# Kernel optimization log

Measured on AMD Instinct MI355X. Metric: run time of the kernel, lower is better.

The kernel has to match this reference:

```python
import jax, jax.numpy as jnp
import numpy as np

B, T, I, H = 64, 512, 512, 512

def setup_inputs() -> dict:
    key = jax.random.key(0)
    ks = jax.random.split(key, 13)
    s = 0.02
    return {
        'inputs': jax.random.normal(ks[0], (B, T, I), dtype=jnp.float32),
        'W_i': jax.random.normal(ks[1], (I, H), dtype=jnp.float32) * s,
        'W_f': jax.random.normal(ks[2], (I, H), dtype=jnp.float32) * s,
        'W_o': jax.random.normal(ks[3], (I, H), dtype=jnp.float32) * s,
        'W_c': jax.random.normal(ks[4], (I, H), dtype=jnp.float32) * s,
        'U_i': jax.random.normal(ks[5], (H, H), dtype=jnp.float32) * s,
        'U_f': jax.random.normal(ks[6], (H, H), dtype=jnp.float32) * s,
        'U_o': jax.random.normal(ks[7], (H, H), dtype=jnp.float32) * s,
        'U_c': jax.random.normal(ks[8], (H, H), dtype=jnp.float32) * s,
        'b_i': jax.random.normal(ks[9], (1, H), dtype=jnp.float32) * s,
        'b_f': jax.random.normal(ks[10], (1, H), dtype=jnp.float32) * s,
        'b_o': jax.random.normal(ks[11], (1, H), dtype=jnp.float32) * s,
        'b_c': jax.random.normal(ks[12], (1, H), dtype=jnp.float32) * s,
    }

def reference(inputs, W_i, W_f, W_o, W_c, U_i, U_f, U_o, U_c, b_i, b_f, b_o, b_c):
    batch = inputs.shape[0]
    hidden = U_i.shape[0]
    # Precompute input projections for all 4 gates in one fused GEMM: [T, B, 4H]
    W = jnp.concatenate([W_i, W_f, W_o, W_c], axis=1)          # [I, 4H]
    b = jnp.concatenate([b_i, b_f, b_o, b_c], axis=1)          # [1, 4H]
    U = jnp.concatenate([U_i, U_f, U_o, U_c], axis=1)          # [H, 4H]
    x_proj = jnp.einsum('bti,ig->tbg', inputs, W) + b          # [T, B, 4H]

    def step(carry, xg):
        h, c = carry
        g = xg + h @ U                                          # [B, 4H]
        i_g = jax.nn.sigmoid(g[:, 0*hidden:1*hidden])
        f_g = jax.nn.sigmoid(g[:, 1*hidden:2*hidden])
        o_g = jax.nn.sigmoid(g[:, 2*hidden:3*hidden])
        c_t = jnp.tanh(g[:, 3*hidden:4*hidden])
        c = f_g * c + i_g * c_t
        h = o_g * jnp.tanh(c)
        return (h, c), None

    h0 = jnp.zeros((batch, hidden), dtype=inputs.dtype)
    c0 = jnp.zeros((batch, hidden), dtype=inputs.dtype)
    (h, c), _ = jax.lax.scan(step, (h0, c0), x_proj)
    return h
```

## Files before the change

### kernel.cpp

```cpp
#include <hip/hip_runtime.h>
#include <hip/hip_bf16.h>
#include <cstdint>


typedef __bf16 bf16;
typedef __bf16 bf16x8 __attribute__((ext_vector_type(8)));
typedef float floatx4 __attribute__((ext_vector_type(4)));
typedef uint64_t u64;
typedef uint32_t u32;

#define T_STEPS 512

#define XP_OFF     0ull
#define XBF_OFF    134217728ull
#define WCT_OFF    167772160ull
#define USW_OFF    169869312ull
#define BCAT_OFF   171966464ull
#define HBUF_OFF   171974656ull

__device__ inline u32 pack_bf16x2(float a, float b) {
    union { __bf16 h[2]; u32 u; } cv;
    cv.h[0] = (__bf16)a; cv.h[1] = (__bf16)b;
    return cv.u;
}
__device__ inline float bf_lo(u32 w) { return __builtin_bit_cast(float, w << 16); }
__device__ inline float bf_hi(u32 w) { return __builtin_bit_cast(float, w & 0xffff0000u); }

__device__ inline void lgkm_barrier() {
    __atomic_signal_fence(__ATOMIC_SEQ_CST);
    __builtin_amdgcn_s_waitcnt(0xc07f);
    __builtin_amdgcn_s_barrier();
    __atomic_signal_fence(__ATOMIC_SEQ_CST);
}

__global__ void k0a_convert(const float* __restrict__ in, bf16* __restrict__ xbf) {
    int o = blockIdx.x * 256 + threadIdx.x;
    int k = o & 511;
    int r = o >> 9;
    int t = r >> 6, b = r & 63;
    xbf[o] = (bf16)in[(b * 512 + t) * 512 + k];
}

__global__ void k0b_wcat(const float* __restrict__ Wi, const float* __restrict__ Wf,
                         const float* __restrict__ Wo, const float* __restrict__ Wc,
                         const float* __restrict__ bi, const float* __restrict__ bfv,
                         const float* __restrict__ bo, const float* __restrict__ bc,
                         bf16* __restrict__ wct, float* __restrict__ bcat) {
    int o = blockIdx.x * 256 + threadIdx.x;
    int k = o & 511;
    int c = o >> 9;
    int h = c >> 2, g = c & 3;
    const float* W = (g == 0) ? Wi : (g == 1) ? Wf : (g == 2) ? Wo : Wc;
    wct[o] = (bf16)W[k * 512 + h];
    if (o < 2048) {
        int hh = o >> 2, gg = o & 3;
        const float* bv = (gg == 0) ? bi : (gg == 1) ? bfv : (gg == 2) ? bo : bc;
        bcat[o] = bv[hh];
    }
}

__global__ void k0c_uswz(const float* __restrict__ Ui, const float* __restrict__ Uf,
                         const float* __restrict__ Uo, const float* __restrict__ Uc,
                         bf16* __restrict__ usw) {
    int o = blockIdx.x * 256 + threadIdx.x;
    int e  = o & 7;
    int l  = (o >> 3) & 63;
    int ks = (o >> 9) & 15;
    int nt = (o >> 13) & 1;
    int w  = (o >> 14) & 3;
    int s  = o >> 16;
    int k = ks * 32 + (l >> 4) * 8 + e;
    int col_local = (2 * w + nt) * 16 + (l & 15);
    int h = s * 32 + (col_local >> 2);
    int g = col_local & 3;
    const float* U = (g == 0) ? Ui : (g == 1) ? Uf : (g == 2) ? Uo : Uc;
    usw[o] = (bf16)U[k * 512 + h];
}

__launch_bounds__(256, 2)
__global__ void k1_gemm(const bf16* __restrict__ xbf, const bf16* __restrict__ wct,
                        const float* __restrict__ bcat, bf16* __restrict__ xp) {
    __shared__ bf16 As[128 * 40];
    __shared__ bf16 Bs[128 * 40];
    int tid = threadIdx.x;
    int wid = tid >> 6, lane = tid & 63;
    int q = lane >> 4, m = lane & 15;
    int wr = wid >> 1, wc = wid & 1;
    int br = blockIdx.x & 255, bc = blockIdx.x >> 8;

    floatx4 acc[4][4] = {};

    for (int kk = 0; kk < 16; ++kk) {
        #pragma unroll
        for (int cc = 0; cc < 2; ++cc) {
            int ch = tid + cc * 256;
            int row = ch >> 2, part = ch & 3;
            bf16x8 va = *(const bf16x8*)&xbf[(br * 128 + row) * 512 + kk * 32 + part * 8];
            bf16x8 vb = *(const bf16x8*)&wct[(bc * 128 + row) * 512 + kk * 32 + part * 8];
            *(bf16x8*)&As[row * 40 + part * 8] = va;
            *(bf16x8*)&Bs[row * 40 + part * 8] = vb;
        }
        __syncthreads();
        bf16x8 af[4], bfr[4];
        #pragma unroll
        for (int i = 0; i < 4; ++i) {
            af[i]  = *(const bf16x8*)&As[(wr * 64 + i * 16 + m) * 40 + q * 8];
            bfr[i] = *(const bf16x8*)&Bs[(wc * 64 + i * 16 + m) * 40 + q * 8];
        }
        #pragma unroll
        for (int mt = 0; mt < 4; ++mt)
            #pragma unroll
            for (int nt = 0; nt < 4; ++nt)
                acc[mt][nt] = __builtin_amdgcn_mfma_f32_16x16x32_bf16(
                    af[mt], bfr[nt], acc[mt][nt], 0, 0, 0);
        __syncthreads();
    }
    float bias[4];
    #pragma unroll
    for (int nt = 0; nt < 4; ++nt) bias[nt] = bcat[bc * 128 + wc * 64 + nt * 16 + m];
    #pragma unroll
    for (int mt = 0; mt < 4; ++mt) {
        #pragma unroll
        for (int nt = 0; nt < 4; ++nt) {
            u32 p0 = pack_bf16x2(acc[mt][nt][0] + bias[nt], acc[mt][nt][1] + bias[nt]);
            u32 p1 = pack_bf16x2(acc[mt][nt][2] + bias[nt], acc[mt][nt][3] + bias[nt]);
            size_t idx = (((((size_t)(br * 2 + wr) * 4 + mt) * 16 + bc) * 8
                           + wc * 4 + nt) * 64 + lane) * 4;
            uint2 v; v.x = p0; v.y = p1;
            *(uint2*)&xp[idx] = v;
        }
    }
}

__launch_bounds__(256, 1)
__global__ void k2_rec(const bf16* __restrict__ xp, const bf16* __restrict__ usw,
                       u64* __restrict__ hbuf, float* __restrict__ out) {
    __shared__ bf16 h_lds[16 * 520];
    __shared__ float g_lds[16 * 136];
    u32* h32 = (u32*)h_lds;

    int tid = threadIdx.x;
    int wid = tid >> 6, lane = tid & 63;
    int q = lane >> 4, m = lane & 15;
    int bg = blockIdx.x & 3, s = blockIdx.x >> 2;

    bf16x8 bfr[2][16];
    {
        const bf16x8* base = (const bf16x8*)usw;
        #pragma unroll
        for (int nt = 0; nt < 2; ++nt)
            #pragma unroll
            for (int ks = 0; ks < 16; ++ks)
                bfr[nt][ks] = base[(((s * 4 + wid) * 2 + nt) * 16 + ks) * 64 + lane];
    }

    int r = tid >> 4;
    int jc = (tid & 15) * 2;
    float cs0 = 0.f, cs1 = 0.f;

    uint2 vx0, vx1;
    {
        size_t b0 = ((((size_t)bg * 16 + s) * 8 + wid * 2) * 64 + lane) * 4;
        vx0 = *(const uint2*)&xp[b0];
        vx1 = *(const uint2*)&xp[b0 + 256];
    }

    for (int t = 0; t < T_STEPS; ++t) {
        floatx4 acc[2];

        acc[0][0] = bf_lo(vx0.x); acc[0][1] = bf_hi(vx0.x);
        acc[0][2] = bf_lo(vx0.y); acc[0][3] = bf_hi(vx0.y);
        acc[1][0] = bf_lo(vx1.x); acc[1][1] = bf_hi(vx1.x);
        acc[1][2] = bf_lo(vx1.y); acc[1][3] = bf_hi(vx1.y);

        if (t > 0) {
            __atomic_signal_fence(__ATOMIC_SEQ_CST);
            __builtin_amdgcn_s_sleep(8);
            __atomic_signal_fence(__ATOMIC_SEQ_CST);

            const u64* rb = hbuf + ((size_t)((t - 1) & 1) * 4 + bg) * 4096;
            u32 tg = (u32)t;
            u64 w[16];
            #pragma unroll
            for (int i = 0; i < 16; ++i)
                w[i] = __hip_atomic_load(rb + tid + 256 * i, __ATOMIC_RELAXED,
                                         __HIP_MEMORY_SCOPE_AGENT);
            for (;;) {
                bool ok = true;
                #pragma unroll
                for (int i = 0; i < 16; ++i) ok &= ((u32)(w[i] >> 32) == tg);
                if (ok) break;
                #pragma unroll
                for (int i = 0; i < 16; ++i)
                    w[i] = __hip_atomic_load(rb + tid + 256 * i, __ATOMIC_RELAXED,
                                             __HIP_MEMORY_SCOPE_AGENT);
            }
            #pragma unroll
            for (int i = 0; i < 16; ++i)
                h32[i * 260 + tid] = (u32)w[i];
            lgkm_barrier();
            #pragma unroll
            for (int ks = 0; ks < 16; ++ks) {
                bf16x8 af = *(const bf16x8*)&h_lds[m * 520 + ks * 32 + q * 8];
                acc[0] = __builtin_amdgcn_mfma_f32_16x16x32_bf16(af, bfr[0][ks], acc[0], 0, 0, 0);
                acc[1] = __builtin_amdgcn_mfma_f32_16x16x32_bf16(af, bfr[1][ks], acc[1], 0, 0, 0);
            }
        }

        if (t + 1 < T_STEPS) {
            size_t b0 = (((((size_t)(t + 1) * 4 + bg) * 16 + s) * 8 + wid * 2) * 64 + lane) * 4;
            vx0 = *(const uint2*)&xp[b0];
            vx1 = *(const uint2*)&xp[b0 + 256];
        }

        #pragma unroll
        for (int nt = 0; nt < 2; ++nt) {
            int col = (2 * wid + nt) * 16 + m;
            #pragma unroll
            for (int rr = 0; rr < 4; ++rr)
                g_lds[(q * 4 + rr) * 136 + col] = acc[nt][rr];
        }
        lgkm_barrier();

        floatx4 ga = *(const floatx4*)&g_lds[r * 136 + jc * 4];
        floatx4 gb = *(const floatx4*)&g_lds[r * 136 + jc * 4 + 4];
        float h0, h1;
        {
            float ig = 1.f / (1.f + __expf(-ga[0]));
            float fg = 1.f / (1.f + __expf(-ga[1]));
            float og = 1.f / (1.f + __expf(-ga[2]));
            float th = 1.f - 2.f / (__expf(2.f * ga[3]) + 1.f);
            cs0 = fg * cs0 + ig * th;
            h0 = og * (1.f - 2.f / (__expf(2.f * cs0) + 1.f));
        }
        {
            float ig = 1.f / (1.f + __expf(-gb[0]));
            float fg = 1.f / (1.f + __expf(-gb[1]));
            float og = 1.f / (1.f + __expf(-gb[2]));
            float th = 1.f - 2.f / (__expf(2.f * gb[3]) + 1.f);
            cs1 = fg * cs1 + ig * th;
            h1 = og * (1.f - 2.f / (__expf(2.f * cs1) + 1.f));
        }
        u64 word = ((u64)(u32)(t + 1) << 32) | (u64)pack_bf16x2(h0, h1);
        __hip_atomic_store(hbuf + (((size_t)(t & 1) * 4 + bg) * 16 + r) * 256
                                + s * 16 + (tid & 15),
                           word, __ATOMIC_RELAXED, __HIP_MEMORY_SCOPE_AGENT);
        if (t == T_STEPS - 1) {
            out[(bg * 16 + r) * 512 + s * 32 + jc]     = h0;
            out[(bg * 16 + r) * 512 + s * 32 + jc + 1] = h1;
        }
    }
}

extern "C" void kernel_launch(void* const* d_in, const int* in_sizes, int n_in,
                              void* d_out, int out_size, void* d_ws, size_t ws_size,
                              hipStream_t stream) {
    const float* inp = (const float*)d_in[0];
    const float* Wi  = (const float*)d_in[1];
    const float* Wf  = (const float*)d_in[2];
    const float* Wo  = (const float*)d_in[3];
    const float* Wc  = (const float*)d_in[4];
    const float* Ui  = (const float*)d_in[5];
    const float* Uf  = (const float*)d_in[6];
    const float* Uo  = (const float*)d_in[7];
    const float* Uc  = (const float*)d_in[8];
    const float* bi  = (const float*)d_in[9];
    const float* bfv = (const float*)d_in[10];
    const float* bo  = (const float*)d_in[11];
    const float* bc  = (const float*)d_in[12];

    char* ws = (char*)d_ws;
    bf16*  xp    = (bf16*)(ws + XP_OFF);
    bf16*  xbf   = (bf16*)(ws + XBF_OFF);
    bf16*  wct   = (bf16*)(ws + WCT_OFF);
    bf16*  usw   = (bf16*)(ws + USW_OFF);
    float* bcat  = (float*)(ws + BCAT_OFF);
    u64*   hbuf  = (u64*)(ws + HBUF_OFF);

    k0a_convert<<<65536, 256, 0, stream>>>(inp, xbf);
    k0b_wcat<<<4096, 256, 0, stream>>>(Wi, Wf, Wo, Wc, bi, bfv, bo, bc, wct, bcat);
    k0c_uswz<<<4096, 256, 0, stream>>>(Ui, Uf, Uo, Uc, usw);
    k1_gemm<<<4096, 256, 0, stream>>>(xbf, wct, bcat, xp);
    k2_rec<<<64, 256, 0, stream>>>(xp, usw, hbuf, (float*)d_out);
}
```

Measured before the change: 1.426 ms.

## Poll hidden state with sc0 inline-asm loads and fall back to an agent-scope mirror buffer

The recurrent kernel now waits for other blocks' hidden state with a tight polling loop. The loop uses inline-asm global loads carrying the sc0 cache bit and a very short sleep. If the data does not arrive within a bounded number of tries, the block permanently switches to the old sleep-and-atomic-load path on a second mirrored buffer. Each step now stores h twice (a plain store plus an atomic store to the mirror). The grid is doubled so that, with half the blocks exiting at once, the remaining 64 blocks are likely spread across different XCDs or CUs. This adds store traffic and depends on cache-coherence behaviour of sc0 loads across XCDs, which may be fragile.

```diff
diff --git a/kernel.cpp b/kernel.cpp
--- a/kernel.cpp
+++ b/kernel.cpp
@@ -10,6 +10,7 @@
 typedef uint32_t u32;
 
 #define T_STEPS 512
+#define FAST_TRIES 512
 
 #define XP_OFF     0ull
 #define XBF_OFF    134217728ull
@@ -17,6 +18,7 @@
 #define USW_OFF    169869312ull
 #define BCAT_OFF   171966464ull
 #define HBUF_OFF   171974656ull
+#define HBUF2_OFF  172236800ull
 
 __device__ inline u32 pack_bf16x2(float a, float b) {
     union { __bf16 h[2]; u32 u; } cv;
@@ -132,9 +134,45 @@
     }
 }
 
+#define POLL_ISSUE(base_)                                                         \
+    asm volatile(                                                                 \
+        "global_load_dwordx2 %[w0],  %[o0], %[sb] sc0\n\t"                        \
+        "global_load_dwordx2 %[w1],  %[o0], %[sb] offset:2048 sc0\n\t"            \
+        "global_load_dwordx2 %[w2],  %[o1], %[sb] sc0\n\t"                        \
+        "global_load_dwordx2 %[w3],  %[o1], %[sb] offset:2048 sc0\n\t"            \
+        "global_load_dwordx2 %[w4],  %[o2], %[sb] sc0\n\t"                        \
+        "global_load_dwordx2 %[w5],  %[o2], %[sb] offset:2048 sc0\n\t"            \
+        "global_load_dwordx2 %[w6],  %[o3], %[sb] sc0\n\t"                        \
+        "global_load_dwordx2 %[w7],  %[o3], %[sb] offset:2048 sc0\n\t"            \
+        "global_load_dwordx2 %[w8],  %[o4], %[sb] sc0\n\t"                        \
+        "global_load_dwordx2 %[w9],  %[o4], %[sb] offset:2048 sc0\n\t"            \
+        "global_load_dwordx2 %[w10], %[o5], %[sb] sc0\n\t"                        \
+        "global_load_dwordx2 %[w11], %[o5], %[sb] offset:2048 sc0\n\t"            \
+        "global_load_dwordx2 %[w12], %[o6], %[sb] sc0\n\t"                        \
+        "global_load_dwordx2 %[w13], %[o6], %[sb] offset:2048 sc0\n\t"            \
+        "global_load_dwordx2 %[w14], %[o7], %[sb] sc0\n\t"                        \
+        "global_load_dwordx2 %[w15], %[o7], %[sb] offset:2048 sc0\n\t"            \
+        "s_waitcnt vmcnt(0)"                                                      \
+        : [w0] "=&v"(w[0]),  [w1] "=&v"(w[1]),  [w2] "=&v"(w[2]),                 \
+          [w3] "=&v"(w[3]),  [w4] "=&v"(w[4]),  [w5] "=&v"(w[5]),                 \
+          [w6] "=&v"(w[6]),  [w7] "=&v"(w[7]),  [w8] "=&v"(w[8]),                 \
+          [w9] "=&v"(w[9]),  [w10] "=&v"(w[10]), [w11] "=&v"(w[11]),              \
+          [w12] "=&v"(w[12]), [w13] "=&v"(w[13]), [w14] "=&v"(w[14]),             \
+          [w15] "=&v"(w[15])                                                      \
+        : [o0] "v"(voff[0]), [o1] "v"(voff[1]), [o2] "v"(voff[2]),                \
+          [o3] "v"(voff[3]), [o4] "v"(voff[4]), [o5] "v"(voff[5]),                \
+          [o6] "v"(voff[6]), [o7] "v"(voff[7]), [sb] "s"(base_)                   \
+        : "memory")
+
 __launch_bounds__(256, 1)
 __global__ void k2_rec(const bf16* __restrict__ xp, const bf16* __restrict__ usw,
-                       u64* __restrict__ hbuf, float* __restrict__ out) {
+                       u64* __restrict__ hbuf, u64* __restrict__ hbuf2,
+                       float* __restrict__ out) {
+    int bid = blockIdx.x;
+    if ((bid & 7) >= 4) return;
+    int bg = bid & 7;
+    int s  = bid >> 3;
+
     __shared__ bf16 h_lds[16 * 520];
     __shared__ float g_lds[16 * 136];
     u32* h32 = (u32*)h_lds;
@@ -142,7 +180,6 @@
     int tid = threadIdx.x;
     int wid = tid >> 6, lane = tid & 63;
     int q = lane >> 4, m = lane & 15;
-    int bg = blockIdx.x & 3, s = blockIdx.x >> 2;
 
     bf16x8 bfr[2][16];
     {
@@ -157,6 +194,12 @@
     int r = tid >> 4;
     int jc = (tid & 15) * 2;
     float cs0 = 0.f, cs1 = 0.f;
+
+    u32 voff[8];
+    #pragma unroll
+    for (int j = 0; j < 8; ++j) voff[j] = (u32)(tid * 8 + j * 4096);
+
+    bool fast_mode = true;
 
     uint2 vx0, vx1;
     {
@@ -174,26 +217,45 @@
         acc[1][2] = bf_lo(vx1.y); acc[1][3] = bf_hi(vx1.y);
 
         if (t > 0) {
-            __atomic_signal_fence(__ATOMIC_SEQ_CST);
-            __builtin_amdgcn_s_sleep(8);
-            __atomic_signal_fence(__ATOMIC_SEQ_CST);
-
-            const u64* rb = hbuf + ((size_t)((t - 1) & 1) * 4 + bg) * 4096;
+            u64 w[16];
             u32 tg = (u32)t;
-            u64 w[16];
-            #pragma unroll
-            for (int i = 0; i < 16; ++i)
-                w[i] = __hip_atomic_load(rb + tid + 256 * i, __ATOMIC_RELAXED,
-                                         __HIP_MEMORY_SCOPE_AGENT);
-            for (;;) {
-                bool ok = true;
-                #pragma unroll
-                for (int i = 0; i < 16; ++i) ok &= ((u32)(w[i] >> 32) == tg);
-                if (ok) break;
+            bool have = false;
+            size_t roff = ((size_t)((t - 1) & 1) * 4 + bg) * 4096;
+
+            if (fast_mode) {
+                u64 rbase = (u64)(uintptr_t)(hbuf + roff);
+                int tries = FAST_TRIES;
+                POLL_ISSUE(rbase);
+                for (;;) {
+                    bool ok = true;
+                    #pragma unroll
+                    for (int i = 0; i < 16; ++i) ok &= ((u32)(w[i] >> 32) == tg);
+                    if (ok) { have = true; break; }
+                    if (--tries == 0) break;
+                    __builtin_amdgcn_s_sleep(1);
+                    POLL_ISSUE(rbase);
+                }
+                if (!have) fast_mode = false;
+            }
+            if (!have) {
+                __atomic_signal_fence(__ATOMIC_SEQ_CST);
+                __builtin_amdgcn_s_sleep(8);
+                __atomic_signal_fence(__ATOMIC_SEQ_CST);
+                const u64* rb = hbuf2 + roff;
                 #pragma unroll
                 for (int i = 0; i < 16; ++i)
                     w[i] = __hip_atomic_load(rb + tid + 256 * i, __ATOMIC_RELAXED,
                                              __HIP_MEMORY_SCOPE_AGENT);
+                for (;;) {
+                    bool ok = true;
+                    #pragma unroll
+                    for (int i = 0; i < 16; ++i) ok &= ((u32)(w[i] >> 32) == tg);
+                    if (ok) break;
+                    #pragma unroll
+                    for (int i = 0; i < 16; ++i)
+                        w[i] = __hip_atomic_load(rb + tid + 256 * i, __ATOMIC_RELAXED,
+                                                 __HIP_MEMORY_SCOPE_AGENT);
+                }
             }
             #pragma unroll
             for (int i = 0; i < 16; ++i)
@@ -242,9 +304,11 @@
             h1 = og * (1.f - 2.f / (__expf(2.f * cs1) + 1.f));
         }
         u64 word = ((u64)(u32)(t + 1) << 32) | (u64)pack_bf16x2(h0, h1);
-        __hip_atomic_store(hbuf + (((size_t)(t & 1) * 4 + bg) * 16 + r) * 256
-                                + s * 16 + (tid & 15),
-                           word, __ATOMIC_RELAXED, __HIP_MEMORY_SCOPE_AGENT);
+        size_t widx = (((size_t)(t & 1) * 4 + bg) * 16 + r) * 256
+                      + s * 16 + (tid & 15);
+        hbuf[widx] = word;
+        __hip_atomic_store(hbuf2 + widx, word, __ATOMIC_RELAXED,
+                           __HIP_MEMORY_SCOPE_AGENT);
         if (t == T_STEPS - 1) {
             out[(bg * 16 + r) * 512 + s * 32 + jc]     = h0;
             out[(bg * 16 + r) * 512 + s * 32 + jc + 1] = h1;
@@ -276,10 +340,11 @@
     bf16*  usw   = (bf16*)(ws + USW_OFF);
     float* bcat  = (float*)(ws + BCAT_OFF);
     u64*   hbuf  = (u64*)(ws + HBUF_OFF);
+    u64*   hbuf2 = (u64*)(ws + HBUF2_OFF);
 
     k0a_convert<<<65536, 256, 0, stream>>>(inp, xbf);
     k0b_wcat<<<4096, 256, 0, stream>>>(Wi, Wf, Wo, Wc, bi, bfv, bo, bc, wct, bcat);
     k0c_uswz<<<4096, 256, 0, stream>>>(Ui, Uf, Uo, Uc, usw);
     k1_gemm<<<4096, 256, 0, stream>>>(xbf, wct, bcat, xp);
-    k2_rec<<<64, 256, 0, stream>>>(xp, usw, hbuf, (float*)d_out);
-}
+    k2_rec<<<128, 256, 0, stream>>>(xp, usw, hbuf, hbuf2, (float*)d_out);
+}
```

Result: slower. 4.114 ms (+188.4%).

## Use per-wave gate slabs, double-buffered swizzled h LDS, drop a block barrier

Applied to the files above, without the earlier changes.

Each wave now writes its own gate outputs into a private LDS slab and computes its own cell updates, so the second block-wide barrier per timestep becomes a wave-local LDS fence. The h buffer in LDS is double-buffered by timestep parity, which makes it safe to drop that barrier, and it uses an XOR swizzle instead of padding to avoid bank conflicts. Work per thread is remapped to match, and the hbuf store and output indices change accordingly. The aim is to shorten the serial per-step critical path of the recurrence, at the risk of getting the new index mapping wrong.

```diff
diff --git a/kernel.cpp b/kernel.cpp
--- a/kernel.cpp
+++ b/kernel.cpp
@@ -30,6 +30,13 @@
     __atomic_signal_fence(__ATOMIC_SEQ_CST);
     __builtin_amdgcn_s_waitcnt(0xc07f);
     __builtin_amdgcn_s_barrier();
+    __atomic_signal_fence(__ATOMIC_SEQ_CST);
+}
+
+__device__ inline void wave_lds_fence() {
+    __atomic_signal_fence(__ATOMIC_SEQ_CST);
+    __builtin_amdgcn_s_waitcnt(0xc07f);
+    __builtin_amdgcn_sched_barrier(0);
     __atomic_signal_fence(__ATOMIC_SEQ_CST);
 }
 
@@ -135,9 +142,8 @@
 __launch_bounds__(256, 1)
 __global__ void k2_rec(const bf16* __restrict__ xp, const bf16* __restrict__ usw,
                        u64* __restrict__ hbuf, float* __restrict__ out) {
-    __shared__ bf16 h_lds[16 * 520];
-    __shared__ float g_lds[16 * 136];
-    u32* h32 = (u32*)h_lds;
+    __shared__ u32 h_sh[2][16 * 256];
+    __shared__ float g_slab[4][16 * 36];
 
     int tid = threadIdx.x;
     int wid = tid >> 6, lane = tid & 63;
@@ -154,9 +160,13 @@
                 bfr[nt][ks] = base[(((s * 4 + wid) * 2 + nt) * 16 + ks) * 64 + lane];
     }
 
-    int r = tid >> 4;
-    int jc = (tid & 15) * 2;
+    int r2 = lane >> 2;
+    int kk2 = lane & 3;
     float cs0 = 0.f, cs1 = 0.f;
+
+    int wc = tid >> 2, wk = tid & 3;
+
+    float* gs = &g_slab[wid][0];
 
     uint2 vx0, vx1;
     {
@@ -195,13 +205,15 @@
                     w[i] = __hip_atomic_load(rb + tid + 256 * i, __ATOMIC_RELAXED,
                                              __HIP_MEMORY_SCOPE_AGENT);
             }
+            u32* hp = &h_sh[(t & 1) ^ 1][0];
             #pragma unroll
             for (int i = 0; i < 16; ++i)
-                h32[i * 260 + tid] = (u32)w[i];
+                hp[i * 256 + ((wc ^ (i & 7)) << 2) + wk] = (u32)w[i];
             lgkm_barrier();
+            const bf16* hbs = (const bf16*)hp;
             #pragma unroll
             for (int ks = 0; ks < 16; ++ks) {
-                bf16x8 af = *(const bf16x8*)&h_lds[m * 520 + ks * 32 + q * 8];
+                bf16x8 af = *(const bf16x8*)&hbs[m * 512 + (((4 * ks + q) ^ (m & 7)) << 3)];
                 acc[0] = __builtin_amdgcn_mfma_f32_16x16x32_bf16(af, bfr[0][ks], acc[0], 0, 0, 0);
                 acc[1] = __builtin_amdgcn_mfma_f32_16x16x32_bf16(af, bfr[1][ks], acc[1], 0, 0, 0);
             }
@@ -214,16 +226,14 @@
         }
 
         #pragma unroll
-        for (int nt = 0; nt < 2; ++nt) {
-            int col = (2 * wid + nt) * 16 + m;
+        for (int nt = 0; nt < 2; ++nt)
             #pragma unroll
             for (int rr = 0; rr < 4; ++rr)
-                g_lds[(q * 4 + rr) * 136 + col] = acc[nt][rr];
-        }
-        lgkm_barrier();
-
-        floatx4 ga = *(const floatx4*)&g_lds[r * 136 + jc * 4];
-        floatx4 gb = *(const floatx4*)&g_lds[r * 136 + jc * 4 + 4];
+                gs[(q * 4 + rr) * 36 + nt * 16 + m] = acc[nt][rr];
+        wave_lds_fence();
+
+        floatx4 ga = *(const floatx4*)&gs[r2 * 36 + kk2 * 8];
+        floatx4 gb = *(const floatx4*)&gs[r2 * 36 + kk2 * 8 + 4];
         float h0, h1;
         {
             float ig = 1.f / (1.f + __expf(-ga[0]));
@@ -242,12 +252,13 @@
             h1 = og * (1.f - 2.f / (__expf(2.f * cs1) + 1.f));
         }
         u64 word = ((u64)(u32)(t + 1) << 32) | (u64)pack_bf16x2(h0, h1);
-        __hip_atomic_store(hbuf + (((size_t)(t & 1) * 4 + bg) * 16 + r) * 256
-                                + s * 16 + (tid & 15),
+        __hip_atomic_store(hbuf + (((size_t)(t & 1) * 4 + bg) * 16 + r2) * 256
+                                + s * 16 + wid * 4 + kk2,
                            word, __ATOMIC_RELAXED, __HIP_MEMORY_SCOPE_AGENT);
         if (t == T_STEPS - 1) {
-            out[(bg * 16 + r) * 512 + s * 32 + jc]     = h0;
-            out[(bg * 16 + r) * 512 + s * 32 + jc + 1] = h1;
+            int u0 = s * 32 + wid * 8 + kk2 * 2;
+            out[(bg * 16 + r2) * 512 + u0]     = h0;
+            out[(bg * 16 + r2) * 512 + u0 + 1] = h1;
         }
     }
 }
```

Result: no change. 1.426 ms (-0.0%).
